# Optimization experiments

Measured on AMD Instinct MI355X. Metric: run time of the kernel, lower is better.

Reference implementation:

```python
import jax, jax.numpy as jnp
import numpy as np

B, D, L = 16384, 1024, 4


def setup_inputs() -> dict:
    key = jax.random.key(0)
    ks = jax.random.split(key, 5)
    scale = 1.0 / np.sqrt(D)
    x = jax.random.normal(ks[0], (B, D), dtype=jnp.float32)
    # torch nn.Linear default init: U(-1/sqrt(fan_in), 1/sqrt(fan_in))
    Ws = jax.random.uniform(ks[1], (L, D, D), jnp.float32, -scale, scale)
    bs = jax.random.uniform(ks[2], (L, D), jnp.float32, -scale, scale)
    Wo = jax.random.uniform(ks[3], (D, D), jnp.float32, -scale, scale)
    bo = jax.random.uniform(ks[4], (D,), jnp.float32, -scale, scale)
    return {"x": x, "Ws": Ws, "bs": bs, "Wo": Wo, "bo": bo}


def reference(x, Ws, bs, Wo, bo):
    # torch: matmul(x[:, :, None], x[:, None, :]).sum(2) == x * x.sum(-1, keepdims=True)
    interactions = jax.nn.relu(x * jnp.sum(x, axis=-1, keepdims=True))  # (B, D)
    h = x
    for i in range(L):  # fixed small layer count
        h = jax.nn.relu(h @ Ws[i].T + bs[i])  # torch Linear: y = x W^T + b
    out = ((h + interactions) * 0.5) @ Wo.T + bo
    return out
```

## Files before the change

### kernel.cpp

```cpp
#include <hip/hip_runtime.h>


#define DDIM 1024
#define BROWS 16384

typedef __attribute__((ext_vector_type(8))) short s8v;
typedef __attribute__((ext_vector_type(4))) float f4v;

__device__ __forceinline__ unsigned short f2bf(float f) {
    unsigned int u = __float_as_uint(f);
    u += 0x7fffu + ((u >> 16) & 1u);
    return (unsigned short)(u >> 16);
}
__device__ __forceinline__ float bf2f(unsigned short u) {
    return __uint_as_float(((unsigned int)u) << 16);
}
__device__ __forceinline__ void gld16(const void* g, void* l) {
    __builtin_amdgcn_global_load_lds(
        (const __attribute__((address_space(1))) unsigned int*)g,
        (__attribute__((address_space(3))) unsigned int*)l, 16, 0, 0);
}

__global__ __launch_bounds__(256) void prep_cvt_kernel(
    const float* __restrict__ x,  const float* __restrict__ Ws,
    const float* __restrict__ Wo, unsigned short* __restrict__ xb,
    unsigned short* __restrict__ wb, float* __restrict__ rowsum)
{
    const int t = threadIdx.x;
    if (blockIdx.x < BROWS) {
        const int row = blockIdx.x;
        const float4 v = *(const float4*)(x + (size_t)row * DDIM + t * 4);
        ushort4 o;
        o.x = f2bf(v.x); o.y = f2bf(v.y); o.z = f2bf(v.z); o.w = f2bf(v.w);
        *(ushort4*)(xb + (size_t)row * DDIM + t * 4) = o;
        float s = v.x + v.y + v.z + v.w;
        #pragma unroll
        for (int off = 32; off > 0; off >>= 1) s += __shfl_down(s, off, 64);
        __shared__ float red[4];
        const int wave = t >> 6, lane = t & 63;
        if (lane == 0) red[wave] = s;
        __syncthreads();
        if (t == 0) rowsum[row] = red[0] + red[1] + red[2] + red[3];
    } else {
        const int base = (blockIdx.x - BROWS) * 1024;
        #pragma unroll
        for (int j = 0; j < 4; ++j) {
            const int idx = base + j * 256 + t;
            const float4 v = (idx < 4 * 262144) ? ((const float4*)Ws)[idx]
                                                : ((const float4*)Wo)[idx - 4 * 262144];
            ushort4 o;
            o.x = f2bf(v.x); o.y = f2bf(v.y); o.z = f2bf(v.z); o.w = f2bf(v.w);
            ((ushort4*)wb)[idx] = o;
        }
    }
}

template <int MODE>
__global__ __launch_bounds__(256, 3) void gemm_bt(
    const unsigned short* __restrict__ A,
    const unsigned short* __restrict__ Bw,
    const float* __restrict__ bias,
    void* __restrict__ out,
    const unsigned short* __restrict__ xb,
    const float* __restrict__ rowsum)
{
    constexpr int K = DDIM, N = DDIM;
    __shared__ unsigned short smem[4][128 * 32];

    const int t = threadIdx.x;
    const int wave = t >> 6, lane = t & 63;
    const int wm = wave & 1, wn = wave >> 1;
    const int rowBase = blockIdx.x * 128;
    const int colBase = blockIdx.y * 128;

    f4v acc[4][4] = {};
    const int c0r = t >> 2, c0k = (t & 3) * 8;
    const int mrow = lane & 15;
    const int quad = lane >> 4;
    const int koff = quad * 8;

    for (int kt = 0; kt < K; kt += 64) {
        if (kt) __syncthreads();
        const unsigned short* a0 = A  + (size_t)(rowBase + c0r) * K + kt + c0k;
        const unsigned short* b0 = Bw + (size_t)(colBase + c0r) * K + kt + c0k;
        gld16(a0,               (char*)smem[0] + t * 16);
        gld16(a0 + 64 * K,      (char*)smem[0] + (t + 256) * 16);
        gld16(b0,               (char*)smem[2] + t * 16);
        gld16(b0 + 64 * K,      (char*)smem[2] + (t + 256) * 16);
        gld16(a0 + 32,          (char*)smem[1] + t * 16);
        gld16(a0 + 64 * K + 32, (char*)smem[1] + (t + 256) * 16);
        gld16(b0 + 32,          (char*)smem[3] + t * 16);
        gld16(b0 + 64 * K + 32, (char*)smem[3] + (t + 256) * 16);
        __syncthreads();
        #pragma unroll
        for (int s = 0; s < 2; ++s) {
            s8v af[4], bfr[4];
            #pragma unroll
            for (int mi = 0; mi < 4; ++mi)
                af[mi] = *(const s8v*)&smem[s][(wm * 64 + mi * 16 + mrow) * 32 + koff];
            #pragma unroll
            for (int ni = 0; ni < 4; ++ni)
                bfr[ni] = *(const s8v*)&smem[2 + s][(wn * 64 + ni * 16 + mrow) * 32 + koff];
            #pragma unroll
            for (int mi = 0; mi < 4; ++mi)
                #pragma unroll
                for (int ni = 0; ni < 4; ++ni)
                    acc[mi][ni] = __builtin_amdgcn_mfma_f32_16x16x32_bf16(
                        af[mi], bfr[ni], acc[mi][ni], 0, 0, 0);
        }
    }

    if (MODE == 2) {
        float* sCf = (float*)smem;
        float* o = (float*)out;
        #pragma unroll 1
        for (int half = 0; half < 2; ++half) {
            __syncthreads();
            if (wm == half) {
                #pragma unroll
                for (int ni = 0; ni < 4; ++ni) {
                    const int n = wn * 64 + ni * 16 + mrow;
                    const float bv = bias[colBase + n];
                    #pragma unroll
                    for (int mi = 0; mi < 4; ++mi)
                        #pragma unroll
                        for (int r = 0; r < 4; ++r)
                            sCf[(mi * 16 + quad * 4 + r) * 128 + n] = acc[mi][ni][r] + bv;
                }
            }
            __syncthreads();
            #pragma unroll
            for (int i = 0; i < 8; ++i) {
                const int idx = t + i * 256;
                const int row = idx >> 5, ch = idx & 31;
                const float4 v = ((const float4*)sCf)[idx];
                ((float4*)(o + (size_t)(rowBase + half * 64 + row) * N + colBase))[ch] = v;
            }
        }
    } else {
        __syncthreads();
        unsigned short* sC = (unsigned short*)smem;
        #pragma unroll
        for (int ni = 0; ni < 4; ++ni) {
            const int n = wn * 64 + ni * 16 + mrow;
            const float bv = bias[colBase + n];
            #pragma unroll
            for (int mi = 0; mi < 4; ++mi)
                #pragma unroll
                for (int r = 0; r < 4; ++r) {
                    const int row = wm * 64 + mi * 16 + quad * 4 + r;
                    float v = acc[mi][ni][r] + bv;
                    v = v > 0.f ? v : 0.f;
                    sC[row * 128 + n] = f2bf(v);
                }
        }
        __syncthreads();
        unsigned short* o16 = (unsigned short*)out;
        #pragma unroll
        for (int i = 0; i < 8; ++i) {
            const int idx = t + i * 256;
            const int row = idx >> 4, ch = idx & 15;
            s8v c = *(const s8v*)&sC[row * 128 + ch * 8];
            if (MODE == 1) {
                const float rsv = rowsum[rowBase + row];
                const s8v xv = *(const s8v*)&xb[(size_t)(rowBase + row) * DDIM + colBase + ch * 8];
                #pragma unroll
                for (int j = 0; j < 8; ++j) {
                    float it = bf2f((unsigned short)xv[j]) * rsv;
                    it = it > 0.f ? it : 0.f;
                    c[j] = (short)f2bf(0.5f * (bf2f((unsigned short)c[j]) + it));
                }
            }
            *(s8v*)&o16[(size_t)(rowBase + row) * DDIM + colBase + ch * 8] = c;
        }
    }
}

extern "C" void kernel_launch(void* const* d_in, const int* in_sizes, int n_in,
                              void* d_out, int out_size, void* d_ws, size_t ws_size,
                              hipStream_t stream) {
    const float* x  = (const float*)d_in[0];
    const float* Ws = (const float*)d_in[1];
    const float* bs = (const float*)d_in[2];
    const float* Wo = (const float*)d_in[3];
    const float* bo = (const float*)d_in[4];
    float* out = (float*)d_out;

    char* ws = (char*)d_ws;
    unsigned short* xb  = (unsigned short*)(ws);
    unsigned short* h0  = (unsigned short*)(ws + 33554432);
    unsigned short* h1  = (unsigned short*)(ws + 67108864);
    unsigned short* wb  = (unsigned short*)(ws + 100663296);
    float*          rsm = (float*)(ws + 111149056);

    prep_cvt_kernel<<<BROWS + 1280, 256, 0, stream>>>(x, Ws, Wo, xb, wb, rsm);

    const size_t WSZ = (size_t)DDIM * DDIM;
    dim3 g(BROWS / 128, DDIM / 128);
    gemm_bt<0><<<g, 256, 0, stream>>>(xb, wb,           bs,            h0, nullptr, nullptr);
    gemm_bt<0><<<g, 256, 0, stream>>>(h0, wb + 1 * WSZ, bs + 1 * DDIM, h1, nullptr, nullptr);
    gemm_bt<0><<<g, 256, 0, stream>>>(h1, wb + 2 * WSZ, bs + 2 * DDIM, h0, nullptr, nullptr);
    gemm_bt<1><<<g, 256, 0, stream>>>(h0, wb + 3 * WSZ, bs + 3 * DDIM, h1, xb, rsm);
    gemm_bt<2><<<g, 256, 0, stream>>>(h1, wb + 4 * WSZ, bo,            out, nullptr, nullptr);
}
```

Baseline: 366.5 us.

## Rewrite GEMM as 256x256-tile, 8-wave kernel with swizzled LDS and interleaved prefetch

Replaces the 128x128, 4-wave GEMM with a 256x256 tile per 512-thread block. Each wave now computes a 128x64 sub-tile. LDS is double-buffered in 64-wide K halves with an XOR swizzle to avoid bank conflicts. Global-to-LDS loads for upcoming K slices are issued between MFMA groups, with explicit vmcnt/lgkmcnt waits and s_setprio raising priority around the MFMA bursts. The aim is to overlap memory with compute, remove the load-then-sync stall of the old loop, and raise arithmetic intensity per byte loaded. The cost is more registers and barriers per block and only 256 blocks per GEMM, which could leave the GPU underfilled.

```diff
diff --git a/kernel.cpp b/kernel.cpp
--- a/kernel.cpp
+++ b/kernel.cpp
@@ -3,6 +3,7 @@
 
 #define DDIM 1024
 #define BROWS 16384
+#define NIT 8
 
 typedef __attribute__((ext_vector_type(8))) short s8v;
 typedef __attribute__((ext_vector_type(4))) float f4v;
@@ -55,8 +56,48 @@
     }
 }
 
+#define MF(a, b, c) __builtin_amdgcn_mfma_f32_16x16x32_bf16(a, b, c, 0, 0, 0)
+#define BAR()   __builtin_amdgcn_s_barrier()
+#define LGKM0() asm volatile("s_waitcnt lgkmcnt(0)" ::: "memory")
+#define VMC(n)  asm volatile("s_waitcnt vmcnt(" #n ")" ::: "memory")
+
+#define SWOFF(lr, cc) ((lr) * 128 + ((((cc) ^ ((lr) & 7))) << 4))
+
+#define SH(src, dst) {                                              \
+    gld16((src) + soff,                   (char*)(dst) + t * 16);   \
+    gld16((src) + soff + (size_t)64 * K,  (char*)(dst) + t * 16 + 8192); }
+
+#define READ_A(P, m0) {                                                               \
+    af[0][0] = *(const s8v*)((const char*)(P) + SWOFF((m0) * 16 + mrow,      quad));      \
+    af[0][1] = *(const s8v*)((const char*)(P) + SWOFF((m0) * 16 + mrow,      4 + quad));  \
+    af[1][0] = *(const s8v*)((const char*)(P) + SWOFF((m0) * 16 + 16 + mrow, quad));      \
+    af[1][1] = *(const s8v*)((const char*)(P) + SWOFF((m0) * 16 + 16 + mrow, 4 + quad)); }
+
+#define READ_B(P) {                                                                   \
+    bfr[0][0] = *(const s8v*)((const char*)(P) + SWOFF(bl + mrow,      quad));            \
+    bfr[0][1] = *(const s8v*)((const char*)(P) + SWOFF(bl + mrow,      4 + quad));        \
+    bfr[1][0] = *(const s8v*)((const char*)(P) + SWOFF(bl + 16 + mrow, quad));            \
+    bfr[1][1] = *(const s8v*)((const char*)(P) + SWOFF(bl + 16 + mrow, 4 + quad));        \
+    bfr[2][0] = *(const s8v*)((const char*)(P) + SWOFF(bl + 32 + mrow, quad));            \
+    bfr[2][1] = *(const s8v*)((const char*)(P) + SWOFF(bl + 32 + mrow, 4 + quad));        \
+    bfr[3][0] = *(const s8v*)((const char*)(P) + SWOFF(bl + 48 + mrow, quad));            \
+    bfr[3][1] = *(const s8v*)((const char*)(P) + SWOFF(bl + 48 + mrow, 4 + quad)); }
+
+#define MMA8(m0, s) {                                              \
+    acc[m0][0]       = MF(af[0][s], bfr[0][s], acc[m0][0]);        \
+    acc[m0][1]       = MF(af[0][s], bfr[1][s], acc[m0][1]);        \
+    acc[m0][2]       = MF(af[0][s], bfr[2][s], acc[m0][2]);        \
+    acc[m0][3]       = MF(af[0][s], bfr[3][s], acc[m0][3]);        \
+    acc[(m0) + 1][0] = MF(af[1][s], bfr[0][s], acc[(m0) + 1][0]);  \
+    acc[(m0) + 1][1] = MF(af[1][s], bfr[1][s], acc[(m0) + 1][1]);  \
+    acc[(m0) + 1][2] = MF(af[1][s], bfr[2][s], acc[(m0) + 1][2]);  \
+    acc[(m0) + 1][3] = MF(af[1][s], bfr[3][s], acc[(m0) + 1][3]); }
+
+#define MMA16(m0) { __builtin_amdgcn_s_setprio(1); MMA8(m0, 0) MMA8(m0, 1) \
+                    __builtin_amdgcn_s_setprio(0); }
+
 template <int MODE>
-__global__ __launch_bounds__(256, 3) void gemm_bt(
+__global__ __launch_bounds__(512, 2) void gemm256(
     const unsigned short* __restrict__ A,
     const unsigned short* __restrict__ Bw,
     const float* __restrict__ bias,
@@ -65,49 +106,84 @@
     const float* __restrict__ rowsum)
 {
     constexpr int K = DDIM, N = DDIM;
-    __shared__ unsigned short smem[4][128 * 32];
+    __shared__ unsigned short smem[2][2][2][128 * 64];
 
     const int t = threadIdx.x;
-    const int wave = t >> 6, lane = t & 63;
-    const int wm = wave & 1, wn = wave >> 1;
-    const int rowBase = blockIdx.x * 128;
-    const int colBase = blockIdx.y * 128;
-
-    f4v acc[4][4] = {};
-    const int c0r = t >> 2, c0k = (t & 3) * 8;
+    const int lane = t & 63;
+    const int wid  = t >> 6;
+    const int wr   = wid >> 2;
+    const int wc   = wid & 3;
     const int mrow = lane & 15;
     const int quad = lane >> 4;
-    const int koff = quad * 8;
-
-    for (int kt = 0; kt < K; kt += 64) {
-        if (kt) __syncthreads();
-        const unsigned short* a0 = A  + (size_t)(rowBase + c0r) * K + kt + c0k;
-        const unsigned short* b0 = Bw + (size_t)(colBase + c0r) * K + kt + c0k;
-        gld16(a0,               (char*)smem[0] + t * 16);
-        gld16(a0 + 64 * K,      (char*)smem[0] + (t + 256) * 16);
-        gld16(b0,               (char*)smem[2] + t * 16);
-        gld16(b0 + 64 * K,      (char*)smem[2] + (t + 256) * 16);
-        gld16(a0 + 32,          (char*)smem[1] + t * 16);
-        gld16(a0 + 64 * K + 32, (char*)smem[1] + (t + 256) * 16);
-        gld16(b0 + 32,          (char*)smem[3] + t * 16);
-        gld16(b0 + 64 * K + 32, (char*)smem[3] + (t + 256) * 16);
-        __syncthreads();
-        #pragma unroll
-        for (int s = 0; s < 2; ++s) {
-            s8v af[4], bfr[4];
-            #pragma unroll
-            for (int mi = 0; mi < 4; ++mi)
-                af[mi] = *(const s8v*)&smem[s][(wm * 64 + mi * 16 + mrow) * 32 + koff];
-            #pragma unroll
-            for (int ni = 0; ni < 4; ++ni)
-                bfr[ni] = *(const s8v*)&smem[2 + s][(wn * 64 + ni * 16 + mrow) * 32 + koff];
-            #pragma unroll
-            for (int mi = 0; mi < 4; ++mi)
-                #pragma unroll
-                for (int ni = 0; ni < 4; ++ni)
-                    acc[mi][ni] = __builtin_amdgcn_mfma_f32_16x16x32_bf16(
-                        af[mi], bfr[ni], acc[mi][ni], 0, 0, 0);
-        }
+    const int rowBase = blockIdx.x * 256;
+    const int colBase = blockIdx.y * 256;
+
+    const unsigned short* const Ab0 = A  + (size_t)rowBase * K;
+    const unsigned short* const Ab1 = Ab0 + (size_t)128 * K;
+    const unsigned short* const Bb0 = Bw + (size_t)colBase * K;
+    const unsigned short* const Bb1 = Bb0 + (size_t)128 * K;
+
+    const int srow = t >> 3;
+    const size_t soff = (size_t)srow * K + (size_t)(((t & 7) ^ (srow & 7)) * 8);
+
+    unsigned short* const a00 = &smem[0][0][0][0];
+    unsigned short* const a01 = &smem[0][0][1][0];
+    unsigned short* const a10 = &smem[0][1][0][0];
+    unsigned short* const a11 = &smem[0][1][1][0];
+    unsigned short* const b00 = &smem[1][0][0][0];
+    unsigned short* const b01 = &smem[1][0][1][0];
+    unsigned short* const b10 = &smem[1][1][0][0];
+    unsigned short* const b11 = &smem[1][1][1][0];
+
+    const unsigned short* const aR0 = wr ? a01 : a00;
+    const unsigned short* const aR1 = wr ? a11 : a10;
+    const unsigned short* const bR0 = (wc >> 1) ? b01 : b00;
+    const unsigned short* const bR1 = (wc >> 1) ? b11 : b10;
+    const int bl = (wc & 1) * 64;
+
+    f4v acc[8][4] = {};
+    s8v af[2][2], bfr[4][2];
+
+    SH(Ab0,      a00); SH(Ab1,      a01);
+    SH(Bb0,      b00); SH(Bb1,      b01);
+    SH(Bb0 + 64, b10); SH(Bb1 + 64, b11);
+    VMC(4);
+    BAR();
+
+    #pragma unroll 1
+    for (int it = 0; it < NIT; ++it) {
+        const int ka = it * 128, kb = ka + 64;
+        const bool more = it < NIT - 1;
+
+        READ_B(bR0); READ_A(aR0, 0);
+        SH(Ab0 + kb, a10);
+        BAR(); LGKM0(); MMA16(0); BAR();
+        READ_A(aR0, 2);
+        SH(Ab1 + kb, a11);
+        BAR(); LGKM0(); MMA16(2); BAR();
+        READ_A(aR0, 4);
+        if (more) SH(Bb0 + ka + 128, b00);
+        BAR(); LGKM0(); MMA16(4); BAR();
+        READ_A(aR0, 6);
+        if (more) SH(Bb1 + ka + 128, b01);
+        BAR(); LGKM0(); MMA16(6);
+        if (more) { VMC(4); } else { VMC(0); }
+        BAR();
+
+        READ_B(bR1); READ_A(aR1, 0);
+        if (more) SH(Ab0 + ka + 128, a00);
+        BAR(); LGKM0(); MMA16(0); BAR();
+        READ_A(aR1, 2);
+        if (more) SH(Ab1 + ka + 128, a01);
+        BAR(); LGKM0(); MMA16(2); BAR();
+        READ_A(aR1, 4);
+        if (more) SH(Bb0 + kb + 128, b10);
+        BAR(); LGKM0(); MMA16(4); BAR();
+        READ_A(aR1, 6);
+        if (more) SH(Bb1 + kb + 128, b11);
+        BAR(); LGKM0(); MMA16(6);
+        if (more) { VMC(4); }
+        BAR();
     }
 
     if (MODE == 2) {
@@ -116,25 +192,25 @@
         #pragma unroll 1
         for (int half = 0; half < 2; ++half) {
             __syncthreads();
-            if (wm == half) {
+            if (wr == half) {
                 #pragma unroll
                 for (int ni = 0; ni < 4; ++ni) {
-                    const int n = wn * 64 + ni * 16 + mrow;
+                    const int n = wc * 64 + ni * 16 + mrow;
                     const float bv = bias[colBase + n];
                     #pragma unroll
-                    for (int mi = 0; mi < 4; ++mi)
+                    for (int mi = 0; mi < 8; ++mi)
                         #pragma unroll
                         for (int r = 0; r < 4; ++r)
-                            sCf[(mi * 16 + quad * 4 + r) * 128 + n] = acc[mi][ni][r] + bv;
+                            sCf[(mi * 16 + quad * 4 + r) * 256 + n] = acc[mi][ni][r] + bv;
                 }
             }
             __syncthreads();
             #pragma unroll
-            for (int i = 0; i < 8; ++i) {
-                const int idx = t + i * 256;
-                const int row = idx >> 5, ch = idx & 31;
+            for (int p = 0; p < 16; ++p) {
+                const int idx = t + p * 512;
+                const int row = idx >> 6, ch = idx & 63;
                 const float4 v = ((const float4*)sCf)[idx];
-                ((float4*)(o + (size_t)(rowBase + half * 64 + row) * N + colBase))[ch] = v;
+                *(float4*)(o + (size_t)(rowBase + half * 128 + row) * N + colBase + ch * 4) = v;
             }
         }
     } else {
@@ -142,33 +218,33 @@
         unsigned short* sC = (unsigned short*)smem;
         #pragma unroll
         for (int ni = 0; ni < 4; ++ni) {
-            const int n = wn * 64 + ni * 16 + mrow;
+            const int n = wc * 64 + ni * 16 + mrow;
             const float bv = bias[colBase + n];
             #pragma unroll
-            for (int mi = 0; mi < 4; ++mi)
+            for (int mi = 0; mi < 8; ++mi)
                 #pragma unroll
                 for (int r = 0; r < 4; ++r) {
-                    const int row = wm * 64 + mi * 16 + quad * 4 + r;
+                    const int row = wr * 128 + mi * 16 + quad * 4 + r;
                     float v = acc[mi][ni][r] + bv;
                     v = v > 0.f ? v : 0.f;
-                    sC[row * 128 + n] = f2bf(v);
+                    sC[row * 256 + n] = f2bf(v);
                 }
         }
         __syncthreads();
         unsigned short* o16 = (unsigned short*)out;
         #pragma unroll
-        for (int i = 0; i < 8; ++i) {
-            const int idx = t + i * 256;
-            const int row = idx >> 4, ch = idx & 15;
-            s8v c = *(const s8v*)&sC[row * 128 + ch * 8];
+        for (int p = 0; p < 16; ++p) {
+            const int idx = t + p * 512;
+            const int row = idx >> 5, ch = idx & 31;
+            s8v c = *(const s8v*)&sC[row * 256 + ch * 8];
             if (MODE == 1) {
                 const float rsv = rowsum[rowBase + row];
                 const s8v xv = *(const s8v*)&xb[(size_t)(rowBase + row) * DDIM + colBase + ch * 8];
                 #pragma unroll
                 for (int j = 0; j < 8; ++j) {
-                    float it = bf2f((unsigned short)xv[j]) * rsv;
-                    it = it > 0.f ? it : 0.f;
-                    c[j] = (short)f2bf(0.5f * (bf2f((unsigned short)c[j]) + it));
+                    float itv = bf2f((unsigned short)xv[j]) * rsv;
+                    itv = itv > 0.f ? itv : 0.f;
+                    c[j] = (short)f2bf(0.5f * (bf2f((unsigned short)c[j]) + itv));
                 }
             }
             *(s8v*)&o16[(size_t)(rowBase + row) * DDIM + colBase + ch * 8] = c;
@@ -196,10 +272,10 @@
     prep_cvt_kernel<<<BROWS + 1280, 256, 0, stream>>>(x, Ws, Wo, xb, wb, rsm);
 
     const size_t WSZ = (size_t)DDIM * DDIM;
-    dim3 g(BROWS / 128, DDIM / 128);
-    gemm_bt<0><<<g, 256, 0, stream>>>(xb, wb,           bs,            h0, nullptr, nullptr);
-    gemm_bt<0><<<g, 256, 0, stream>>>(h0, wb + 1 * WSZ, bs + 1 * DDIM, h1, nullptr, nullptr);
-    gemm_bt<0><<<g, 256, 0, stream>>>(h1, wb + 2 * WSZ, bs + 2 * DDIM, h0, nullptr, nullptr);
-    gemm_bt<1><<<g, 256, 0, stream>>>(h0, wb + 3 * WSZ, bs + 3 * DDIM, h1, xb, rsm);
-    gemm_bt<2><<<g, 256, 0, stream>>>(h1, wb + 4 * WSZ, bo,            out, nullptr, nullptr);
-}
+    dim3 g(BROWS / 256, DDIM / 256);
+    gemm256<0><<<g, 512, 0, stream>>>(xb, wb,           bs,            h0, nullptr, nullptr);
+    gemm256<0><<<g, 512, 0, stream>>>(h0, wb + 1 * WSZ, bs + 1 * DDIM, h1, nullptr, nullptr);
+    gemm256<0><<<g, 512, 0, stream>>>(h1, wb + 2 * WSZ, bs + 2 * DDIM, h0, nullptr, nullptr);
+    gemm256<1><<<g, 512, 0, stream>>>(h0, wb + 3 * WSZ, bs + 3 * DDIM, h1, xb, rsm);
+    gemm256<2><<<g, 512, 0, stream>>>(h1, wb + 4 * WSZ, bo,            out, nullptr, nullptr);
+}
```

Measured after the change: 317.5 us. -13.4%, faster.

## Fuse all five layers into one row-resident kernel with LDS-held activations

Applied to the files above, without the earlier changes.

Replaces the five separate tiled GEMM launches with one kernel in which each 512-thread block owns 64 rows. The block keeps the full 64x1024 bf16 activation tile in swizzled LDS across all layers and streams weight fragments straight from global memory into registers. This removes the intermediate h0/h1 global round trips and four kernel launches. The cost is that every block rereads all weights from global or L2 with no LDS reuse, only 256 blocks run (about one per CU), and the final layer writes fp32 output with scattered non-coalesced stores.

```diff
diff --git a/kernel.cpp b/kernel.cpp
--- a/kernel.cpp
+++ b/kernel.cpp
@@ -55,123 +55,107 @@
     }
 }
 
-template <int MODE>
-__global__ __launch_bounds__(256, 3) void gemm_bt(
-    const unsigned short* __restrict__ A,
-    const unsigned short* __restrict__ Bw,
-    const float* __restrict__ bias,
-    void* __restrict__ out,
-    const unsigned short* __restrict__ xb,
-    const float* __restrict__ rowsum)
+#define MF(a, b, c) __builtin_amdgcn_mfma_f32_16x16x32_bf16(a, b, c, 0, 0, 0)
+
+#define LOADB(B, kk) { _Pragma("unroll") for (int ni = 0; ni < 8; ++ni)   \
+    B[ni] = *(const s8v*)(wB + (size_t)ni * 16384 + (kk) * 32); }
+
+#define LOADA(A, kk) { _Pragma("unroll") for (int mi = 0; mi < 4; ++mi)   \
+    A[mi] = *(const s8v*)((const char*)hL + (mi * 16 + l15) * 2048         \
+              + (((((kk) * 4 + quad)) ^ (l15 & 7)) << 4)); }
+
+#define MSTEP(A, B) { __builtin_amdgcn_s_setprio(1);                       \
+    _Pragma("unroll") for (int ni = 0; ni < 8; ++ni)                       \
+      _Pragma("unroll") for (int mi = 0; mi < 4; ++mi)                     \
+        acc[mi][ni] = MF(A[mi], B[ni], acc[mi][ni]);                       \
+    __builtin_amdgcn_s_setprio(0); }
+
+__global__ __launch_bounds__(512, 2) void deepfm_rowres(
+    const unsigned short* __restrict__ xb, const unsigned short* __restrict__ wb,
+    const float* __restrict__ bs, const float* __restrict__ bo,
+    const float* __restrict__ rsm, float* __restrict__ out)
 {
-    constexpr int K = DDIM, N = DDIM;
-    __shared__ unsigned short smem[4][128 * 32];
+    __shared__ unsigned short hL[64 * 1024];
 
     const int t = threadIdx.x;
-    const int wave = t >> 6, lane = t & 63;
-    const int wm = wave & 1, wn = wave >> 1;
-    const int rowBase = blockIdx.x * 128;
-    const int colBase = blockIdx.y * 128;
+    const int lane = t & 63;
+    const int wid  = t >> 6;
+    const int l15  = lane & 15;
+    const int quad = lane >> 4;
+    const int row0 = blockIdx.x * 64;
+    const int colS = wid * 128;
 
-    f4v acc[4][4] = {};
-    const int c0r = t >> 2, c0k = (t & 3) * 8;
-    const int mrow = lane & 15;
-    const int quad = lane >> 4;
-    const int koff = quad * 8;
+    #pragma unroll
+    for (int i = 0; i < 16; ++i) {
+        const int d = t + i * 512;
+        const int r = d >> 7, ch = d & 127;
+        gld16(xb + (size_t)(row0 + r) * DDIM + (size_t)((ch ^ (r & 7)) * 8),
+              (char*)hL + (size_t)d * 16);
+    }
+    asm volatile("s_waitcnt vmcnt(0)" ::: "memory");
+    __syncthreads();
 
-    for (int kt = 0; kt < K; kt += 64) {
-        if (kt) __syncthreads();
-        const unsigned short* a0 = A  + (size_t)(rowBase + c0r) * K + kt + c0k;
-        const unsigned short* b0 = Bw + (size_t)(colBase + c0r) * K + kt + c0k;
-        gld16(a0,               (char*)smem[0] + t * 16);
-        gld16(a0 + 64 * K,      (char*)smem[0] + (t + 256) * 16);
-        gld16(b0,               (char*)smem[2] + t * 16);
-        gld16(b0 + 64 * K,      (char*)smem[2] + (t + 256) * 16);
-        gld16(a0 + 32,          (char*)smem[1] + t * 16);
-        gld16(a0 + 64 * K + 32, (char*)smem[1] + (t + 256) * 16);
-        gld16(b0 + 32,          (char*)smem[3] + t * 16);
-        gld16(b0 + 64 * K + 32, (char*)smem[3] + (t + 256) * 16);
-        __syncthreads();
+    f4v acc[4][8];
+    s8v a0[4], a1[4], b0[8], b1[8];
+
+    #pragma unroll 1
+    for (int l = 0; l < 5; ++l) {
+        const unsigned short* const wB =
+            wb + (size_t)l * DDIM * DDIM + (size_t)(colS + l15) * DDIM + quad * 8;
+        const float* const bias = (l == 4) ? bo : (bs + (size_t)l * DDIM);
+
         #pragma unroll
-        for (int s = 0; s < 2; ++s) {
-            s8v af[4], bfr[4];
+        for (int mi = 0; mi < 4; ++mi)
             #pragma unroll
-            for (int mi = 0; mi < 4; ++mi)
-                af[mi] = *(const s8v*)&smem[s][(wm * 64 + mi * 16 + mrow) * 32 + koff];
+            for (int ni = 0; ni < 8; ++ni)
+                acc[mi][ni] = (f4v){0.f, 0.f, 0.f, 0.f};
+
+        LOADB(b0, 0); LOADA(a0, 0);
+        #pragma unroll 1
+        for (int kk = 0; kk < 32; kk += 2) {
+            LOADB(b1, kk + 1); LOADA(a1, kk + 1);
+            MSTEP(a0, b0);
+            if (kk + 2 < 32) { LOADB(b0, kk + 2); LOADA(a0, kk + 2); }
+            MSTEP(a1, b1);
+        }
+
+        if (l == 4) {
             #pragma unroll
-            for (int ni = 0; ni < 4; ++ni)
-                bfr[ni] = *(const s8v*)&smem[2 + s][(wn * 64 + ni * 16 + mrow) * 32 + koff];
+            for (int ni = 0; ni < 8; ++ni) {
+                const int col = colS + ni * 16 + l15;
+                const float bv = bias[col];
+                #pragma unroll
+                for (int mi = 0; mi < 4; ++mi)
+                    #pragma unroll
+                    for (int r = 0; r < 4; ++r) {
+                        const int row = mi * 16 + quad * 4 + r;
+                        out[(size_t)(row0 + row) * DDIM + col] = acc[mi][ni][r] + bv;
+                    }
+            }
+        } else {
+            __syncthreads();
             #pragma unroll
-            for (int mi = 0; mi < 4; ++mi)
+            for (int ni = 0; ni < 8; ++ni) {
+                const int col = colS + ni * 16 + l15;
+                const float bv = bias[col];
                 #pragma unroll
-                for (int ni = 0; ni < 4; ++ni)
-                    acc[mi][ni] = __builtin_amdgcn_mfma_f32_16x16x32_bf16(
-                        af[mi], bfr[ni], acc[mi][ni], 0, 0, 0);
-        }
-    }
-
-    if (MODE == 2) {
-        float* sCf = (float*)smem;
-        float* o = (float*)out;
-        #pragma unroll 1
-        for (int half = 0; half < 2; ++half) {
-            __syncthreads();
-            if (wm == half) {
-                #pragma unroll
-                for (int ni = 0; ni < 4; ++ni) {
-                    const int n = wn * 64 + ni * 16 + mrow;
-                    const float bv = bias[colBase + n];
+                for (int mi = 0; mi < 4; ++mi)
                     #pragma unroll
-                    for (int mi = 0; mi < 4; ++mi)
-                        #pragma unroll
-                        for (int r = 0; r < 4; ++r)
-                            sCf[(mi * 16 + quad * 4 + r) * 128 + n] = acc[mi][ni][r] + bv;
-                }
+                    for (int r = 0; r < 4; ++r) {
+                        const int row = mi * 16 + quad * 4 + r;
+                        float v = acc[mi][ni][r] + bv;
+                        v = v > 0.f ? v : 0.f;
+                        if (l == 3) {
+                            const float rv = rsm[row0 + row];
+                            float itv = bf2f(xb[(size_t)(row0 + row) * DDIM + col]) * rv;
+                            itv = itv > 0.f ? itv : 0.f;
+                            v = 0.5f * (v + itv);
+                        }
+                        *(unsigned short*)((char*)hL + row * 2048
+                            + (((col >> 3) ^ (row & 7)) << 4) + (col & 7) * 2) = f2bf(v);
+                    }
             }
             __syncthreads();
-            #pragma unroll
-            for (int i = 0; i < 8; ++i) {
-                const int idx = t + i * 256;
-                const int row = idx >> 5, ch = idx & 31;
-                const float4 v = ((const float4*)sCf)[idx];
-                ((float4*)(o + (size_t)(rowBase + half * 64 + row) * N + colBase))[ch] = v;
-            }
-        }
-    } else {
-        __syncthreads();
-        unsigned short* sC = (unsigned short*)smem;
-        #pragma unroll
-        for (int ni = 0; ni < 4; ++ni) {
-            const int n = wn * 64 + ni * 16 + mrow;
-            const float bv = bias[colBase + n];
-            #pragma unroll
-            for (int mi = 0; mi < 4; ++mi)
-                #pragma unroll
-                for (int r = 0; r < 4; ++r) {
-                    const int row = wm * 64 + mi * 16 + quad * 4 + r;
-                    float v = acc[mi][ni][r] + bv;
-                    v = v > 0.f ? v : 0.f;
-                    sC[row * 128 + n] = f2bf(v);
-                }
-        }
-        __syncthreads();
-        unsigned short* o16 = (unsigned short*)out;
-        #pragma unroll
-        for (int i = 0; i < 8; ++i) {
-            const int idx = t + i * 256;
-            const int row = idx >> 4, ch = idx & 15;
-            s8v c = *(const s8v*)&sC[row * 128 + ch * 8];
-            if (MODE == 1) {
-                const float rsv = rowsum[rowBase + row];
-                const s8v xv = *(const s8v*)&xb[(size_t)(rowBase + row) * DDIM + colBase + ch * 8];
-                #pragma unroll
-                for (int j = 0; j < 8; ++j) {
-                    float it = bf2f((unsigned short)xv[j]) * rsv;
-                    it = it > 0.f ? it : 0.f;
-                    c[j] = (short)f2bf(0.5f * (bf2f((unsigned short)c[j]) + it));
-                }
-            }
-            *(s8v*)&o16[(size_t)(rowBase + row) * DDIM + colBase + ch * 8] = c;
         }
     }
 }
@@ -188,18 +172,9 @@
 
     char* ws = (char*)d_ws;
     unsigned short* xb  = (unsigned short*)(ws);
-    unsigned short* h0  = (unsigned short*)(ws + 33554432);
-    unsigned short* h1  = (unsigned short*)(ws + 67108864);
-    unsigned short* wb  = (unsigned short*)(ws + 100663296);
-    float*          rsm = (float*)(ws + 111149056);
+    unsigned short* wb  = (unsigned short*)(ws + 33554432);
+    float*          rsm = (float*)(ws + 44040192);
 
     prep_cvt_kernel<<<BROWS + 1280, 256, 0, stream>>>(x, Ws, Wo, xb, wb, rsm);
-
-    const size_t WSZ = (size_t)DDIM * DDIM;
-    dim3 g(BROWS / 128, DDIM / 128);
-    gemm_bt<0><<<g, 256, 0, stream>>>(xb, wb,           bs,            h0, nullptr, nullptr);
-    gemm_bt<0><<<g, 256, 0, stream>>>(h0, wb + 1 * WSZ, bs + 1 * DDIM, h1, nullptr, nullptr);
-    gemm_bt<0><<<g, 256, 0, stream>>>(h1, wb + 2 * WSZ, bs + 2 * DDIM, h0, nullptr, nullptr);
-    gemm_bt<1><<<g, 256, 0, stream>>>(h0, wb + 3 * WSZ, bs + 3 * DDIM, h1, xb, rsm);
-    gemm_bt<2><<<g, 256, 0, stream>>>(h1, wb + 4 * WSZ, bo,            out, nullptr, nullptr);
+    deepfm_rowres<<<dim3(256), dim3(512), 0, stream>>>(xb, wb, bs, bo, rsm, out);
 }
```

New measurement: 639.5 us. 74.5% more time.
